# Optimization experiments

Hardware: AMD Instinct MI355X
Metric: run time of the kernel (lower is better)

Reference implementation:

```python
import jax, jax.numpy as jnp
import numpy as np

DIM = 512
BATCH = 65536


def setup_inputs() -> dict:
    key = jax.random.key(0)
    k1, k2 = jax.random.split(key)
    pq = jax.random.normal(k1, (BATCH, 2 * DIM), dtype=jnp.float32)
    A = jax.random.normal(k2, (DIM, DIM), dtype=jnp.float32)
    return {"pq": pq, "A": A}


def reference(pq, A):
    # up_or_low == 'up': pterm_i = (A + A^T) @ q_i, qterm = 0
    # npq = [p + pterm, q]
    S = A + A.T  # symmetric (dim, dim)
    p = pq[:, :DIM]
    q = pq[:, DIM:]
    # torch.mv(S, q_i) for every row i  ==  q @ S.T  (single batched matvec/GEMM)
    pterm = jnp.einsum("bd,ed->be", q, S)
    return jnp.concatenate([p + pterm, q], axis=-1)
```

## Files before the change

### kernel.cpp

```cpp
#include <hip/hip_runtime.h>

#define DIM 512
#define BATCH 65536
#define BM 32
#define THREADS 512

typedef float f32x4 __attribute__((ext_vector_type(4)));
typedef float f32x16 __attribute__((ext_vector_type(16)));
typedef __bf16 bf16x8 __attribute__((ext_vector_type(8)));

__device__ __forceinline__ unsigned f2bf(float f) {
    unsigned u = __float_as_uint(f);
    return (u + 0x7FFFu + ((u >> 16) & 1u)) >> 16;
}

__global__ void prep_Sfrag(const float* __restrict__ A, unsigned short* __restrict__ Sf) {
    int idx = blockIdx.x * 256 + threadIdx.x;
    int lane = idx & 63;
    int np   = (idx >> 6) & 15;
    int k0   = idx >> 10;
    int n     = np * 32 + (lane & 31);
    int kbase = k0 * 16 + (lane >> 5) * 8;
    unsigned short tmp[8];
    #pragma unroll
    for (int j = 0; j < 8; ++j) {
        int k = kbase + j;
        tmp[j] = (unsigned short)f2bf(A[n * DIM + k] + A[k * DIM + n]);
    }
    *(uint4*)(Sf + (size_t)idx * 8) = *(const uint4*)tmp;
}

__global__ __launch_bounds__(THREADS, 4)
void gemm_kernel(const float* __restrict__ pq,
                 const unsigned short* __restrict__ Sf,
                 float* __restrict__ out) {
    __shared__ unsigned short qs[BM * DIM];
    const int rb  = blockIdx.x * BM;
    const int tid = threadIdx.x;
    const int wid  = tid >> 6;
    const int lane = tid & 63;
    const int row  = lane & 31;
    const int khalf = lane >> 5;

    #pragma unroll
    for (int i = 0; i < 8; ++i) {
        int flat = (tid + i * THREADS) * 4;
        int r = flat >> 9, c = flat & 511;
        size_t g = (size_t)(rb + r) * 1024 + 512 + c;
        f32x4 v = __builtin_nontemporal_load((const f32x4*)(pq + g));
        __builtin_nontemporal_store(v, (f32x4*)(out + g));
        unsigned lo = f2bf(v.x) | (f2bf(v.y) << 16);
        unsigned hi = f2bf(v.z) | (f2bf(v.w) << 16);
        int bo = (c * 2) ^ ((r & 15) << 4);
        *(uint2*)((char*)qs + r * 1024 + bo) = make_uint2(lo, hi);
    }
    __syncthreads();

    const unsigned short* Sfp = Sf + ((size_t)(wid * 2) * 64 + lane) * 8;
    f32x16 acc0 = {}, acc1 = {};
    bf16x8 a_c  = *(const bf16x8*)((const char*)qs + row * 1024 +
                                   ((khalf * 16) ^ ((row & 15) << 4)));
    bf16x8 b0_c = *(const bf16x8*)(Sfp);
    bf16x8 b1_c = *(const bf16x8*)(Sfp + 512);
    #pragma unroll
    for (int k0 = 0; k0 < 32; ++k0) {
        bf16x8 a_n, b0_n, b1_n;
        if (k0 < 31) {
            int bo = ((k0 + 1) * 32 + khalf * 16) ^ ((row & 15) << 4);
            a_n  = *(const bf16x8*)((const char*)qs + row * 1024 + bo);
            b0_n = *(const bf16x8*)(Sfp + (size_t)(k0 + 1) * 8192);
            b1_n = *(const bf16x8*)(Sfp + (size_t)(k0 + 1) * 8192 + 512);
        }
        acc0 = __builtin_amdgcn_mfma_f32_32x32x16_bf16(a_c, b0_c, acc0, 0, 0, 0);
        acc1 = __builtin_amdgcn_mfma_f32_32x32x16_bf16(a_c, b1_c, acc1, 0, 0, 0);
        if (k0 < 31) { a_c = a_n; b0_c = b0_n; b1_c = b1_n; }
    }

    float* sc = (float*)qs;
    __syncthreads();
    #pragma unroll
    for (int pass = 0; pass < 2; ++pass) {
        const f32x16& ac = pass ? acc1 : acc0;
        #pragma unroll
        for (int reg = 0; reg < 16; ++reg) {
            int r = (reg & 3) + 8 * (reg >> 2) + 4 * khalf;
            sc[r * 256 + wid * 32 + row] = ac[reg];
        }
        __syncthreads();
        #pragma unroll
        for (int j = 0; j < 4; ++j) {
            int c  = tid + j * 512;
            int r  = c >> 6, cc = c & 63;
            int gcol = (cc >> 3) * 64 + (cc & 7) * 4 + pass * 32;
            size_t g = (size_t)(rb + r) * 1024 + gcol;
            f32x4 v  = *(const f32x4*)(sc + r * 256 + cc * 4);
            f32x4 pv = __builtin_nontemporal_load((const f32x4*)(pq + g));
            __builtin_nontemporal_store(pv + v, (f32x4*)(out + g));
        }
        __syncthreads();
    }
}

extern "C" void kernel_launch(void* const* d_in, const int* in_sizes, int n_in,
                              void* d_out, int out_size, void* d_ws, size_t ws_size,
                              hipStream_t stream) {
    const float* pq = (const float*)d_in[0];
    const float* A  = (const float*)d_in[1];
    float* out = (float*)d_out;
    unsigned short* Sf = (unsigned short*)d_ws;

    prep_Sfrag<<<128, 256, 0, stream>>>(A, Sf);
    gemm_kernel<<<BATCH / BM, THREADS, 0, stream>>>(pq, Sf, out);
}
```

Measured before the change: 135.2 us.

## Halve block threads and give each wave four N-tiles for A-fragment reuse

Reduces the workgroup from 8 waves to 4 and has each wave compute four 32x32 output tiles instead of two, so every A fragment read from LDS feeds four MFMAs. The q staging and epilogue loops are adjusted for the smaller thread count, and the column mapping is rewritten to match. This cuts LDS reads of q and the per-block wave count, at the cost of more accumulator and prefetch registers per wave, which may lower occupancy, and fewer waves to hide global latency.

```diff
diff --git a/kernel.cpp b/kernel.cpp
--- a/kernel.cpp
+++ b/kernel.cpp
@@ -3,7 +3,7 @@
 #define DIM 512
 #define BATCH 65536
 #define BM 32
-#define THREADS 512
+#define THREADS 256
 
 typedef float f32x4 __attribute__((ext_vector_type(4)));
 typedef float f32x16 __attribute__((ext_vector_type(16)));
@@ -43,7 +43,7 @@
     const int khalf = lane >> 5;
 
     #pragma unroll
-    for (int i = 0; i < 8; ++i) {
+    for (int i = 0; i < 16; ++i) {
         int flat = (tid + i * THREADS) * 4;
         int r = flat >> 9, c = flat & 511;
         size_t g = (size_t)(rb + r) * 1024 + 512 + c;
@@ -56,44 +56,54 @@
     }
     __syncthreads();
 
-    const unsigned short* Sfp = Sf + ((size_t)(wid * 2) * 64 + lane) * 8;
-    f32x16 acc0 = {}, acc1 = {};
+    const unsigned short* Sfp = Sf + ((size_t)(wid * 4) * 64 + lane) * 8;
+    f32x16 acc0 = {}, acc1 = {}, acc2 = {}, acc3 = {};
     bf16x8 a_c  = *(const bf16x8*)((const char*)qs + row * 1024 +
                                    ((khalf * 16) ^ ((row & 15) << 4)));
     bf16x8 b0_c = *(const bf16x8*)(Sfp);
     bf16x8 b1_c = *(const bf16x8*)(Sfp + 512);
+    bf16x8 b2_c = *(const bf16x8*)(Sfp + 1024);
+    bf16x8 b3_c = *(const bf16x8*)(Sfp + 1536);
     #pragma unroll
     for (int k0 = 0; k0 < 32; ++k0) {
-        bf16x8 a_n, b0_n, b1_n;
+        bf16x8 a_n, b0_n, b1_n, b2_n, b3_n;
         if (k0 < 31) {
             int bo = ((k0 + 1) * 32 + khalf * 16) ^ ((row & 15) << 4);
             a_n  = *(const bf16x8*)((const char*)qs + row * 1024 + bo);
-            b0_n = *(const bf16x8*)(Sfp + (size_t)(k0 + 1) * 8192);
-            b1_n = *(const bf16x8*)(Sfp + (size_t)(k0 + 1) * 8192 + 512);
+            const unsigned short* s = Sfp + (size_t)(k0 + 1) * 8192;
+            b0_n = *(const bf16x8*)(s);
+            b1_n = *(const bf16x8*)(s + 512);
+            b2_n = *(const bf16x8*)(s + 1024);
+            b3_n = *(const bf16x8*)(s + 1536);
         }
         acc0 = __builtin_amdgcn_mfma_f32_32x32x16_bf16(a_c, b0_c, acc0, 0, 0, 0);
         acc1 = __builtin_amdgcn_mfma_f32_32x32x16_bf16(a_c, b1_c, acc1, 0, 0, 0);
-        if (k0 < 31) { a_c = a_n; b0_c = b0_n; b1_c = b1_n; }
+        acc2 = __builtin_amdgcn_mfma_f32_32x32x16_bf16(a_c, b2_c, acc2, 0, 0, 0);
+        acc3 = __builtin_amdgcn_mfma_f32_32x32x16_bf16(a_c, b3_c, acc3, 0, 0, 0);
+        if (k0 < 31) { a_c = a_n; b0_c = b0_n; b1_c = b1_n; b2_c = b2_n; b3_c = b3_n; }
     }
 
     float* sc = (float*)qs;
     __syncthreads();
     #pragma unroll
     for (int pass = 0; pass < 2; ++pass) {
-        const f32x16& ac = pass ? acc1 : acc0;
+        const f32x16& aA = pass ? acc2 : acc0;
+        const f32x16& aB = pass ? acc3 : acc1;
         #pragma unroll
         for (int reg = 0; reg < 16; ++reg) {
             int r = (reg & 3) + 8 * (reg >> 2) + 4 * khalf;
-            sc[r * 256 + wid * 32 + row] = ac[reg];
+            sc[r * 256 + wid * 64 + row]      = aA[reg];
+            sc[r * 256 + wid * 64 + 32 + row] = aB[reg];
         }
         __syncthreads();
         #pragma unroll
-        for (int j = 0; j < 4; ++j) {
-            int c  = tid + j * 512;
+        for (int j = 0; j < 8; ++j) {
+            int c  = tid + j * THREADS;
             int r  = c >> 6, cc = c & 63;
-            int gcol = (cc >> 3) * 64 + (cc & 7) * 4 + pass * 32;
+            int scCol = cc * 4;
+            int gcol  = (scCol >> 6) * 128 + pass * 64 + (scCol & 63);
             size_t g = (size_t)(rb + r) * 1024 + gcol;
-            f32x4 v  = *(const f32x4*)(sc + r * 256 + cc * 4);
+            f32x4 v  = *(const f32x4*)(sc + r * 256 + scCol);
             f32x4 pv = __builtin_nontemporal_load((const f32x4*)(pq + g));
             __builtin_nontemporal_store(pv + v, (f32x4*)(out + g));
         }
```

Result: slower. 144.1 us (+6.5%).
